# Kernel optimization log

Hardware: AMD Instinct MI355X
Metric: run time of the kernel (lower is better)

Reference implementation:

```python
import jax, jax.numpy as jnp
import numpy as np

N = 100000      # nodes
E = 1600000     # edges (avg degree 16)
F_IN = 256      # Data.num_features
H = 128         # hidden_channels
C = 10          # num classes


def setup_inputs() -> dict:
    key = jax.random.key(0)
    ks = jax.random.split(key, 5)
    x = jax.random.normal(ks[0], (N, F_IN), dtype=jnp.float32)
    edge_index = jax.random.randint(ks[1], (2, E), 0, N, dtype=jnp.int32)
    W1 = jax.random.normal(ks[2], (F_IN, H), dtype=jnp.float32) / np.sqrt(F_IN)
    b1 = jnp.zeros((H,), dtype=jnp.float32)
    W2 = jax.random.normal(ks[3], (H, C), dtype=jnp.float32) / np.sqrt(H)
    b2 = jnp.zeros((C,), dtype=jnp.float32)
    return {"x": x, "edge_index": edge_index, "W1": W1, "b1": b1, "W2": W2, "b2": b2}


def _gcn_conv(x, W, b, src, dst, dinv_sqrt):
    # dense transform first (PyG GCNConv order), then normalized gather-scatter
    h = x @ W                                   # [N, out]
    norm = dinv_sqrt[src] * dinv_sqrt[dst]      # [E+N]
    msg = h[src] * norm[:, None]                # [E+N, out]
    out = jax.ops.segment_sum(msg, dst, num_segments=N)
    return out + b


def reference(x, edge_index, W1, b1, W2, b2):
    # add self-loops (GCNConv default)
    loop = jnp.arange(N, dtype=edge_index.dtype)
    src = jnp.concatenate([edge_index[0], loop])
    dst = jnp.concatenate([edge_index[1], loop])
    # symmetric normalization: D^-1/2 (A+I) D^-1/2, degree counted on dst
    deg = jax.ops.segment_sum(jnp.ones_like(dst, dtype=x.dtype), dst, num_segments=N)
    dinv_sqrt = jnp.where(deg > 0, jax.lax.rsqrt(deg), 0.0)
    h = _gcn_conv(x, W1, b1, src, dst, dinv_sqrt)
    h = jax.nn.relu(h)
    h = _gcn_conv(h, W2, b2, src, dst, dinv_sqrt)
    return jax.nn.log_softmax(h, axis=1)
```

## Files before the change

### kernel.cpp

```cpp
#include <hip/hip_runtime.h>
#include <math.h>

#define BLK 256
#define BKT_BITS 8
#define BKT (1<<BKT_BITS)
#define NBMAX 512
#define EB 2048
#define BSTRIDE 8192

typedef __attribute__((ext_vector_type(8))) short bf16x8;
typedef __attribute__((ext_vector_type(4))) float f32x4;

__device__ inline unsigned short f2b(float f){
  union { float f; unsigned int u; } v; v.f = f;
  unsigned int u = v.u;
  return (unsigned short)((u + 0x7FFF + ((u >> 16) & 1)) >> 16);
}
__device__ inline float b2f_lo(unsigned int u){
  union { unsigned int u; float f; } v; v.u = u << 16; return v.f;
}
__device__ inline float b2f_hi(unsigned int u){
  union { unsigned int u; float f; } v; v.u = u & 0xFFFF0000u; return v.f;
}
__device__ inline unsigned pkbf(float lo, float hi){
  unsigned r;
  asm("v_cvt_pk_bf16_f32 %0, %1, %2" : "=v"(r) : "v"(lo), "v"(hi));
  return r;
}


__global__ __launch_bounds__(256)
void binc_wcvt(const int* __restrict__ src, const int* __restrict__ dst,
               int* __restrict__ bcnt, unsigned int* __restrict__ bins,
               const float* __restrict__ W1, unsigned short* __restrict__ W1T,
               int E, int NCB){
  __shared__ int lh[NBMAX];
  __shared__ int lofs[NBMAX];
  __shared__ int lcur[NBMAX];
  __shared__ int gres[NBMAX];
  __shared__ int sscan[256];
  __shared__ __attribute__((aligned(16))) int2 buf[EB];
  int b = blockIdx.x;
  if (b >= NCB){
    int t2 = (b - NCB)*256 + threadIdx.x;
    if (t2 < 256*128){
      int k = t2 >> 7, n = t2 & 127;
      W1T[n*256 + k] = f2b(W1[t2]);
    }
    return;
  }
  int t = threadIdx.x;
  lh[t] = 0; lh[t+256] = 0;
  __syncthreads();
  int base = b*EB;
  #pragma unroll
  for (int k=0;k<EB/1024;k++){
    int idx = base + (k*256 + t)*4;
    if (idx < E){
      int4 d = *(const int4*)(dst + idx);
      atomicAdd(&lh[d.x>>BKT_BITS],1);
      atomicAdd(&lh[d.y>>BKT_BITS],1);
      atomicAdd(&lh[d.z>>BKT_BITS],1);
      atomicAdd(&lh[d.w>>BKT_BITS],1);
    }
  }
  __syncthreads();
  int i0 = 2*t, i1 = 2*t+1;
  int v0 = lh[i0], v1 = lh[i1];
  int tsum = v0+v1;
  sscan[t] = tsum; __syncthreads();
  for (int off=1; off<256; off<<=1){
    int v = (t>=off)? sscan[t-off]:0;
    __syncthreads();
    sscan[t]+=v;
    __syncthreads();
  }
  int run = sscan[t]-tsum;
  lofs[i0] = run;      lofs[i1] = run+v0;
  lcur[i0] = run;      lcur[i1] = run+v0;
  for (int i=t;i<NBMAX;i+=256)
    gres[i] = lh[i] ? (i*BSTRIDE + atomicAdd(&bcnt[i], lh[i])) : 0;
  __syncthreads();
  #pragma unroll
  for (int k=0;k<EB/1024;k++){
    int idx = base + (k*256 + t)*4;
    if (idx < E){
      int4 s4 = *(const int4*)(src + idx);
      int4 d4 = *(const int4*)(dst + idx);
      int p;
      p = atomicAdd(&lcur[d4.x>>BKT_BITS],1); buf[p] = make_int2(s4.x,d4.x);
      p = atomicAdd(&lcur[d4.y>>BKT_BITS],1); buf[p] = make_int2(s4.y,d4.y);
      p = atomicAdd(&lcur[d4.z>>BKT_BITS],1); buf[p] = make_int2(s4.z,d4.z);
      p = atomicAdd(&lcur[d4.w>>BKT_BITS],1); buf[p] = make_int2(s4.w,d4.w);
    }
  }
  __syncthreads();
  int total = E - base; if (total > EB) total = EB;
  for (int i=t; i<total; i+=256){
    int2 pr = buf[i];
    int bb = pr.y>>BKT_BITS;
    bins[gres[bb] + (i - lofs[bb])] = ((unsigned)pr.x << BKT_BITS) | (unsigned)(pr.y & (BKT-1));
  }
}


__global__ __launch_bounds__(512)
void bfill_gemm1(const unsigned int* __restrict__ bins, const int* __restrict__ bcnt,
                 int* __restrict__ rowptr, float* __restrict__ dinv, int* __restrict__ col,
                 const float* __restrict__ X, const unsigned short* __restrict__ W1T,
                 unsigned short* __restrict__ H1B, int N, int NB){
  __shared__ __attribute__((aligned(16))) char smem[64*512*2];
  const int b = blockIdx.x;
  const int t = threadIdx.x;

  if (b < NB){
    int* dcnt  = (int*)smem;
    int* rp    = dcnt + 256;
    int* cur   = rp + 256;
    int* sscan = cur + 256;
    int* sboff = sscan + 256;
    if (t == 0) *sboff = 0;
    if (t < 256) dcnt[t] = 0;
    __syncthreads();
    int partial = 0;
    for (int j=t; j<b; j+=512) partial += bcnt[j];
    if (partial) atomicAdd(sboff, partial);
    __syncthreads();
    int s = *sboff, cnt = bcnt[b];
    const unsigned int* mybins = bins + (size_t)b*BSTRIDE;
    for (int i=t;i<cnt;i+=512) atomicAdd(&dcnt[mybins[i] & (BKT-1)], 1);
    __syncthreads();
    int base = b<<BKT_BITS;
    int node = base + t;
    int d0 = 0, n0 = 0;
    if (t < 256){
      d0 = dcnt[t];
      n0 = (node < N) ? d0+1 : 0;
      sscan[t] = n0;
    }
    __syncthreads();
    for (int off=1; off<256; off<<=1){
      int v = 0;
      if (t < 256 && t >= off) v = sscan[t-off];
      __syncthreads();
      if (t < 256) sscan[t] += v;
      __syncthreads();
    }
    if (t < 256){
      int run = sscan[t]-n0;
      int rp0 = s + base + run;
      rp[t] = rp0; cur[t] = 0;
      if (node < N){
        rowptr[node] = rp0;
        dinv[node] = rsqrtf((float)(d0+1));
        col[rp0 + d0] = node;
        if (node == N-1) rowptr[N] = rp0 + d0 + 1;
      }
    }
    __syncthreads();
    for (int i=t;i<cnt;i+=512){
      unsigned pk = mybins[i];
      int ln = pk & (BKT-1);
      int slot = atomicAdd(&cur[ln], 1);
      col[rp[ln] + slot] = (int)(pk >> BKT_BITS);
    }
    return;
  }

  unsigned short* wsh = (unsigned short*)smem;
  const int bid = b - NB;
  const int wave = t >> 6, lane = t & 63;
  const int quad = lane >> 4, l16 = lane & 15;
  const int M = N;

  #pragma unroll
  for (int f0=0; f0<64; f0+=8){
    int f = f0 + wave;
    int ct = f >> 3, ts = f & 7;
    uint4 v = *(const uint4*)(W1T + (ct*16 + l16)*256 + ts*32 + quad*8);
    *(uint4*)(wsh + f*512 + lane*8) = v;
  }
  __syncthreads();

  const int row0 = bid * 256 + wave * 32;
  int rA = row0 + l16;
  int rB = rA + 16;
  int rAc = (rA < M) ? rA : (M-1);
  int rBc = (rB < M) ? rB : (M-1);
  const float* xA = X + (size_t)rAc*256 + quad*8;
  const float* xB = X + (size_t)rBc*256 + quad*8;

  f32x4 acc[2][8];
  #pragma unroll
  for (int i=0;i<2;i++)
    #pragma unroll
    for (int j=0;j<8;j++) acc[i][j] = (f32x4){0.f,0.f,0.f,0.f};

  float4 pf[2][4];
  #pragma unroll
  for (int s=0;s<2;s++){
    pf[s][0] = *(const float4*)(xA + s*32);
    pf[s][1] = *(const float4*)(xA + s*32 + 4);
    pf[s][2] = *(const float4*)(xB + s*32);
    pf[s][3] = *(const float4*)(xB + s*32 + 4);
  }

  #pragma unroll
  for (int tt=0; tt<8; tt++){
    const int cur2 = tt & 1;
    union { bf16x8 v; unsigned u[4]; } fa, fb;
    fa.u[0] = pkbf(pf[cur2][0].x, pf[cur2][0].y);
    fa.u[1] = pkbf(pf[cur2][0].z, pf[cur2][0].w);
    fa.u[2] = pkbf(pf[cur2][1].x, pf[cur2][1].y);
    fa.u[3] = pkbf(pf[cur2][1].z, pf[cur2][1].w);
    fb.u[0] = pkbf(pf[cur2][2].x, pf[cur2][2].y);
    fb.u[1] = pkbf(pf[cur2][2].z, pf[cur2][2].w);
    fb.u[2] = pkbf(pf[cur2][3].x, pf[cur2][3].y);
    fb.u[3] = pkbf(pf[cur2][3].z, pf[cur2][3].w);
    if (tt < 6){
      pf[cur2][0] = *(const float4*)(xA + (tt+2)*32);
      pf[cur2][1] = *(const float4*)(xA + (tt+2)*32 + 4);
      pf[cur2][2] = *(const float4*)(xB + (tt+2)*32);
      pf[cur2][3] = *(const float4*)(xB + (tt+2)*32 + 4);
    }
    #pragma unroll
    for (int ct=0; ct<8; ct++){
      bf16x8 bf = *(const bf16x8*)(wsh + (ct*8 + tt)*512 + lane*8);
      acc[0][ct] = __builtin_amdgcn_mfma_f32_16x16x32_bf16(fa.v, bf, acc[0][ct], 0, 0, 0);
      acc[1][ct] = __builtin_amdgcn_mfma_f32_16x16x32_bf16(fb.v, bf, acc[1][ct], 0, 0, 0);
    }
  }

  #pragma unroll
  for (int rt=0; rt<2; rt++){
    int rbase = row0 + rt*16 + quad*4;
    #pragma unroll
    for (int rg=0; rg<4; rg++){
      int grow = rbase + rg;
      if (grow < M){
        float dv = dinv[grow];
        #pragma unroll
        for (int ct=0; ct<8; ct++)
          H1B[(size_t)grow*128 + ct*16 + l16] = f2b(dv * acc[rt][ct][rg]);
      }
    }
  }
}


__device__ inline void acc8(float* a, uint4 u){
  a[0]+=b2f_lo(u.x); a[1]+=b2f_hi(u.x); a[2]+=b2f_lo(u.y); a[3]+=b2f_hi(u.y);
  a[4]+=b2f_lo(u.z); a[5]+=b2f_hi(u.z); a[6]+=b2f_lo(u.w); a[7]+=b2f_hi(u.w);
}

__global__ __launch_bounds__(256)
void agg1_kernel(const unsigned short* __restrict__ H1B, const int* __restrict__ rowptr,
                 const int* __restrict__ col, const float* __restrict__ dinv,
                 const float* __restrict__ b1, unsigned int* __restrict__ R1B, int N){
  int node = blockIdx.x * 4 + (threadIdx.x >> 6);
  int lane = threadIdx.x & 63;
  int g   = lane >> 4;
  int l16 = lane & 15;
  if (node >= N) return;
  int s = rowptr[node], e = rowptr[node+1];
  float a[8];
  #pragma unroll
  for (int k=0;k<8;k++) a[k]=0.f;
  const char* hbase = (const char*)H1B + l16*16;
  int j = s;
  for (; j+15 < e; j+=16){
    int c0 = col[j+g], c1 = col[j+4+g], c2 = col[j+8+g], c3 = col[j+12+g];
    uint4 u0 = *(const uint4*)(hbase + (((unsigned)c0) << 8));
    uint4 u1 = *(const uint4*)(hbase + (((unsigned)c1) << 8));
    uint4 u2 = *(const uint4*)(hbase + (((unsigned)c2) << 8));
    uint4 u3 = *(const uint4*)(hbase + (((unsigned)c3) << 8));
    acc8(a, u0); acc8(a, u1); acc8(a, u2); acc8(a, u3);
  }
  for (; j+7 < e; j+=8){
    int c0 = col[j+g], c1 = col[j+4+g];
    uint4 u0 = *(const uint4*)(hbase + (((unsigned)c0) << 8));
    uint4 u1 = *(const uint4*)(hbase + (((unsigned)c1) << 8));
    acc8(a, u0); acc8(a, u1);
  }
  {
    int rem = e - j;
    if (g < rem){
      int c0 = col[j+g];
      uint4 u0 = *(const uint4*)(hbase + (((unsigned)c0) << 8));
      acc8(a, u0);
    }
    if (g+4 < rem){
      int c1 = col[j+4+g];
      uint4 u1 = *(const uint4*)(hbase + (((unsigned)c1) << 8));
      acc8(a, u1);
    }
  }
  #pragma unroll
  for (int k=0;k<8;k++){
    a[k] += __shfl_xor(a[k], 16);
    a[k] += __shfl_xor(a[k], 32);
  }
  if (g == 0){
    float dv = dinv[node];
    float4 bl = *(const float4*)(b1 + l16*8);
    float4 bh = *(const float4*)(b1 + l16*8 + 4);
    float f0, f1;
    unsigned int o0, o1, o2, o3;
    f0 = fmaxf(dv*a[0] + bl.x, 0.f); f1 = fmaxf(dv*a[1] + bl.y, 0.f);
    o0 = (unsigned)f2b(f0) | ((unsigned)f2b(f1) << 16);
    f0 = fmaxf(dv*a[2] + bl.z, 0.f); f1 = fmaxf(dv*a[3] + bl.w, 0.f);
    o1 = (unsigned)f2b(f0) | ((unsigned)f2b(f1) << 16);
    f0 = fmaxf(dv*a[4] + bh.x, 0.f); f1 = fmaxf(dv*a[5] + bh.y, 0.f);
    o2 = (unsigned)f2b(f0) | ((unsigned)f2b(f1) << 16);
    f0 = fmaxf(dv*a[6] + bh.z, 0.f); f1 = fmaxf(dv*a[7] + bh.w, 0.f);
    o3 = (unsigned)f2b(f0) | ((unsigned)f2b(f1) << 16);
    *(uint4*)(R1B + (size_t)node*64 + l16*4) = make_uint4(o0, o1, o2, o3);
  }
}


__global__ __launch_bounds__(256)
void gemm2_kernel(const unsigned int* __restrict__ R1B, const float* __restrict__ W2,
                  const float* __restrict__ dinv, unsigned int* __restrict__ H2B, int M){
  __shared__ float w2s[128*10];
  for (int i = threadIdx.x; i < 128*10; i += blockDim.x) w2s[i] = W2[i];
  __syncthreads();
  int r = blockIdx.x*blockDim.x + threadIdx.x;
  if (r >= M) return;
  float acc[10];
  #pragma unroll
  for (int c=0;c<10;c++) acc[c] = 0.f;
  const unsigned int* row = R1B + (size_t)r*64;
  for (int k=0;k<64;k+=4){
    uint4 u = *(const uint4*)(row + k);
    float f0 = b2f_lo(u.x), f1 = b2f_hi(u.x);
    float f2 = b2f_lo(u.y), f3 = b2f_hi(u.y);
    float f4 = b2f_lo(u.z), f5 = b2f_hi(u.z);
    float f6 = b2f_lo(u.w), f7 = b2f_hi(u.w);
    #pragma unroll
    for (int c=0;c<10;c++){
      acc[c] += f0*w2s[(2*k+0)*10+c] + f1*w2s[(2*k+1)*10+c]
              + f2*w2s[(2*k+2)*10+c] + f3*w2s[(2*k+3)*10+c]
              + f4*w2s[(2*k+4)*10+c] + f5*w2s[(2*k+5)*10+c]
              + f6*w2s[(2*k+6)*10+c] + f7*w2s[(2*k+7)*10+c];
    }
  }
  float dv = dinv[r];
  unsigned int p[5];
  #pragma unroll
  for (int c=0;c<5;c++)
    p[c] = (unsigned)f2b(dv*acc[2*c]) | ((unsigned)f2b(dv*acc[2*c+1]) << 16);
  unsigned int* op = H2B + (size_t)r*8;
  *(uint4*)op = make_uint4(p[0],p[1],p[2],p[3]);
  *(uint4*)(op+4) = make_uint4(p[4],0u,0u,0u);
}


__global__ __launch_bounds__(256)
void agg2_softmax_kernel(const unsigned int* __restrict__ H2B, const int* __restrict__ rowptr,
                         const int* __restrict__ col, const float* __restrict__ dinv,
                         const float* __restrict__ b2, float* __restrict__ out, int N){
  int tid = threadIdx.x;
  int node = blockIdx.x * 16 + (tid >> 4);
  int l16 = tid & 15;
  int g2 = l16 >> 3;
  int l8 = l16 & 7;
  if (node >= N) return;
  int s = rowptr[node], e = rowptr[node+1];
  float aLo = 0.f, aHi = 0.f, bLo = 0.f, bHi = 0.f;
  const unsigned int* hb = H2B + l8;
  int j = s;
  for (; j+3 < e; j += 4){
    unsigned u0 = hb[(size_t)col[j+g2]*8];
    unsigned u1 = hb[(size_t)col[j+2+g2]*8];
    aLo += b2f_lo(u0); aHi += b2f_hi(u0);
    bLo += b2f_lo(u1); bHi += b2f_hi(u1);
  }
  for (; j+1 < e; j += 2){
    unsigned u0 = hb[(size_t)col[j+g2]*8];
    aLo += b2f_lo(u0); aHi += b2f_hi(u0);
  }
  if (j < e && g2 == 0){
    unsigned u0 = hb[(size_t)col[j]*8];
    aLo += b2f_lo(u0); aHi += b2f_hi(u0);
  }
  aLo += bLo; aHi += bHi;
  aLo += __shfl_xor(aLo, 8);
  aHi += __shfl_xor(aHi, 8);
  float dv = dinv[node];
  float2 bb = (l8 < 5) ? *(const float2*)(b2 + 2*l8) : make_float2(0.f, 0.f);
  float c0 = (l8 < 5) ? (dv*aLo + bb.x) : -1e30f;
  float c1 = (l8 < 5) ? (dv*aHi + bb.y) : -1e30f;
  float m = fmaxf(c0, c1);
  m = fmaxf(m, __shfl_xor(m, 1));
  m = fmaxf(m, __shfl_xor(m, 2));
  m = fmaxf(m, __shfl_xor(m, 4));
  float ex = (l8 < 5) ? (expf(c0 - m) + expf(c1 - m)) : 0.f;
  ex += __shfl_xor(ex, 1);
  ex += __shfl_xor(ex, 2);
  ex += __shfl_xor(ex, 4);
  float lg = m + logf(ex);
  if (l8 < 5 && g2 == 0)
    *(float2*)(out + (size_t)node*10 + 2*l8) = make_float2(c0 - lg, c1 - lg);
}


extern "C" void kernel_launch(void* const* d_in, const int* in_sizes, int n_in,
                              void* d_out, int out_size, void* d_ws, size_t ws_size,
                              hipStream_t stream){
  const float* x    = (const float*)d_in[0];
  const int*   ei   = (const int*)d_in[1];
  const float* W1   = (const float*)d_in[2];
  const float* b1   = (const float*)d_in[3];
  const float* W2   = (const float*)d_in[4];
  const float* b2   = (const float*)d_in[5];
  float* out = (float*)d_out;

  const int N = in_sizes[0] / 256;
  const int E = in_sizes[1] / 2;
  const int NNZ = E + N;
  const int* src = ei;
  const int* dst = ei + E;
  const int NB = (N + BKT - 1) >> BKT_BITS;
  const int WB = 128;
  const int GB = (N + 255) / 256;

  char* ws = (char*)d_ws;
  size_t off = 0;
  auto alloc = [&](size_t bytes)->char*{
    char* p = ws + off;
    off = (off + bytes + 255) & ~(size_t)255;
    return p;
  };
  int*   bcnt   = (int*)  alloc((size_t)NBMAX*4);
  float* dinv   = (float*)alloc((size_t)N*4);
  int*   rowptr = (int*)  alloc((size_t)(N+1)*4);
  unsigned int* bins = (unsigned int*)alloc((size_t)NB*BSTRIDE*4);
  int*   col    = (int*)  alloc((size_t)NNZ*4);
  unsigned short* w1t = (unsigned short*)alloc((size_t)128*256*2);
  unsigned short* h1b = (unsigned short*)alloc((size_t)N*128*2);
  unsigned int*   r1b = (unsigned int*)  alloc((size_t)N*64*4);
  unsigned int*   h2b = (unsigned int*)  alloc((size_t)N*8*4);
  (void)ws_size;

  hipMemsetAsync(bcnt, 0, (size_t)NBMAX*4, stream);

  const int NCB = (E + EB - 1) / EB;

  binc_wcvt<<<NCB + WB, 256, 0, stream>>>(src, dst, bcnt, bins, W1, w1t, E, NCB);
  bfill_gemm1<<<NB + GB, 512, 0, stream>>>(bins, bcnt, rowptr, dinv, col, x, w1t, h1b, N, NB);

  agg1_kernel<<<(N+3)/4, 256, 0, stream>>>(h1b, rowptr, col, dinv, b1, r1b, N);
  gemm2_kernel<<<(N+BLK-1)/BLK, BLK, 0, stream>>>(r1b, W2, dinv, h2b, N);
  agg2_softmax_kernel<<<(N+15)/16, BLK, 0, stream>>>(h2b, rowptr, col, dinv, b2, out, N);
}
```

Baseline: 316.1 us.

## Interleave CSR-build and GEMM1 blocks; apply source dinv in aggregation

```diff
diff --git a/kernel.cpp b/kernel.cpp
--- a/kernel.cpp
+++ b/kernel.cpp
@@ -110,10 +110,11 @@
                  const float* __restrict__ X, const unsigned short* __restrict__ W1T,
                  unsigned short* __restrict__ H1B, int N, int NB){
   __shared__ __attribute__((aligned(16))) char smem[64*512*2];
-  const int b = blockIdx.x;
   const int t = threadIdx.x;
-
-  if (b < NB){
+  const int half = blockIdx.x >> 1;
+
+  if (blockIdx.x & 1){
+    const int b = half;
     int* dcnt  = (int*)smem;
     int* rp    = dcnt + 256;
     int* cur   = rp + 256;
@@ -168,7 +169,7 @@
   }
 
   unsigned short* wsh = (unsigned short*)smem;
-  const int bid = b - NB;
+  const int bid = half;
   const int wave = t >> 6, lane = t & 63;
   const int quad = lane >> 4, l16 = lane & 15;
   const int M = N;
@@ -238,19 +239,20 @@
     for (int rg=0; rg<4; rg++){
       int grow = rbase + rg;
       if (grow < M){
-        float dv = dinv[grow];
         #pragma unroll
         for (int ct=0; ct<8; ct++)
-          H1B[(size_t)grow*128 + ct*16 + l16] = f2b(dv * acc[rt][ct][rg]);
+          H1B[(size_t)grow*128 + ct*16 + l16] = f2b(acc[rt][ct][rg]);
       }
     }
   }
 }
 
 
-__device__ inline void acc8(float* a, uint4 u){
-  a[0]+=b2f_lo(u.x); a[1]+=b2f_hi(u.x); a[2]+=b2f_lo(u.y); a[3]+=b2f_hi(u.y);
-  a[4]+=b2f_lo(u.z); a[5]+=b2f_hi(u.z); a[6]+=b2f_lo(u.w); a[7]+=b2f_hi(u.w);
+__device__ inline void acc8s(float* a, uint4 u, float v){
+  a[0]=fmaf(v,b2f_lo(u.x),a[0]); a[1]=fmaf(v,b2f_hi(u.x),a[1]);
+  a[2]=fmaf(v,b2f_lo(u.y),a[2]); a[3]=fmaf(v,b2f_hi(u.y),a[3]);
+  a[4]=fmaf(v,b2f_lo(u.z),a[4]); a[5]=fmaf(v,b2f_hi(u.z),a[5]);
+  a[6]=fmaf(v,b2f_lo(u.w),a[6]); a[7]=fmaf(v,b2f_hi(u.w),a[7]);
 }
 
 __global__ __launch_bounds__(256)
@@ -274,25 +276,27 @@
     uint4 u1 = *(const uint4*)(hbase + (((unsigned)c1) << 8));
     uint4 u2 = *(const uint4*)(hbase + (((unsigned)c2) << 8));
     uint4 u3 = *(const uint4*)(hbase + (((unsigned)c3) << 8));
-    acc8(a, u0); acc8(a, u1); acc8(a, u2); acc8(a, u3);
+    float v0 = dinv[c0], v1 = dinv[c1], v2 = dinv[c2], v3 = dinv[c3];
+    acc8s(a, u0, v0); acc8s(a, u1, v1); acc8s(a, u2, v2); acc8s(a, u3, v3);
   }
   for (; j+7 < e; j+=8){
     int c0 = col[j+g], c1 = col[j+4+g];
     uint4 u0 = *(const uint4*)(hbase + (((unsigned)c0) << 8));
     uint4 u1 = *(const uint4*)(hbase + (((unsigned)c1) << 8));
-    acc8(a, u0); acc8(a, u1);
+    float v0 = dinv[c0], v1 = dinv[c1];
+    acc8s(a, u0, v0); acc8s(a, u1, v1);
   }
   {
     int rem = e - j;
     if (g < rem){
       int c0 = col[j+g];
       uint4 u0 = *(const uint4*)(hbase + (((unsigned)c0) << 8));
-      acc8(a, u0);
+      acc8s(a, u0, dinv[c0]);
     }
     if (g+4 < rem){
       int c1 = col[j+4+g];
       uint4 u1 = *(const uint4*)(hbase + (((unsigned)c1) << 8));
-      acc8(a, u1);
+      acc8s(a, u1, dinv[c1]);
     }
   }
   #pragma unroll
@@ -331,6 +335,7 @@
   #pragma unroll
   for (int c=0;c<10;c++) acc[c] = 0.f;
   const unsigned int* row = R1B + (size_t)r*64;
+  #pragma unroll
   for (int k=0;k<64;k+=4){
     uint4 u = *(const uint4*)(row + k);
     float f0 = b2f_lo(u.x), f1 = b2f_hi(u.x);
@@ -368,8 +373,19 @@
   if (node >= N) return;
   int s = rowptr[node], e = rowptr[node+1];
   float aLo = 0.f, aHi = 0.f, bLo = 0.f, bHi = 0.f;
+  float cLo = 0.f, cHi = 0.f, dLo = 0.f, dHi = 0.f;
   const unsigned int* hb = H2B + l8;
   int j = s;
+  for (; j+7 < e; j += 8){
+    unsigned u0 = hb[(size_t)col[j+g2]*8];
+    unsigned u1 = hb[(size_t)col[j+2+g2]*8];
+    unsigned u2 = hb[(size_t)col[j+4+g2]*8];
+    unsigned u3 = hb[(size_t)col[j+6+g2]*8];
+    aLo += b2f_lo(u0); aHi += b2f_hi(u0);
+    bLo += b2f_lo(u1); bHi += b2f_hi(u1);
+    cLo += b2f_lo(u2); cHi += b2f_hi(u2);
+    dLo += b2f_lo(u3); dHi += b2f_hi(u3);
+  }
   for (; j+3 < e; j += 4){
     unsigned u0 = hb[(size_t)col[j+g2]*8];
     unsigned u1 = hb[(size_t)col[j+2+g2]*8];
@@ -384,7 +400,7 @@
     unsigned u0 = hb[(size_t)col[j]*8];
     aLo += b2f_lo(u0); aHi += b2f_hi(u0);
   }
-  aLo += bLo; aHi += bHi;
+  aLo += bLo + cLo + dLo; aHi += bHi + cHi + dHi;
   aLo += __shfl_xor(aLo, 8);
   aHi += __shfl_xor(aHi, 8);
   float dv = dinv[node];
```

After: 320.4 us. Within noise of the previous version (+1.4%).
